# Optimization experiments

Hardware: AMD Instinct MI355X
Metric: run time of the kernel (lower is better)

Reference implementation:

```python
import jax, jax.numpy as jnp
import numpy as np

B, L, C = 32, 8192, 32
P, S = 16, 8
N = (L - P) // S + 1  # 1023 tokens
K = 16
HID = max(16, 2 * K)  # 32
STD_FLOOR = 0.01


def setup_inputs() -> dict:
    key = jax.random.key(0)
    ks = jax.random.split(key, 8)
    return {
        "x": jax.random.normal(ks[0], (B, L, C), jnp.float32),
        "freq_features": jax.random.normal(ks[1], (B * C, N, K), jnp.float32),
        "alpha_w1": jax.random.normal(ks[2], (K, HID), jnp.float32) * 0.1,
        "alpha_b1": jnp.zeros((HID,), jnp.float32),
        "alpha_w2": jax.random.normal(ks[3], (HID, 1), jnp.float32) * 0.1,
        "alpha_b2": jnp.zeros((1,), jnp.float32),
        "beta_w1": jax.random.normal(ks[4], (K, HID), jnp.float32) * 0.1,
        "beta_b1": jnp.zeros((HID,), jnp.float32),
        "beta_w2": jax.random.normal(ks[5], (HID, 1), jnp.float32) * 0.1,
        "beta_b2": jnp.zeros((1,), jnp.float32),
        "affine_scale": jnp.ones((C,), jnp.float32),
        "affine_bias": jnp.zeros((C,), jnp.float32),
        "n_tokens": N,
    }


def _gate_mlp(ff, w1, b1, w2, b2):
    # Linear -> exact GELU (torch default) -> Linear -> sigmoid, squeeze last dim
    h = jax.nn.gelu(ff @ w1 + b1, approximate=False)
    return jax.nn.sigmoid((h @ w2 + b2)[..., 0])


def reference(x, freq_features, alpha_w1, alpha_b1, alpha_w2, alpha_b2,
              beta_w1, beta_b1, beta_w2, beta_b2, affine_scale, affine_bias,
              n_tokens):
    Bx, Lx, Cx = x.shape
    Nn = n_tokens
    # global stats over time dim (biased var)
    mu_g = jnp.mean(x, axis=1, keepdims=True)                     # [B,1,C]
    var_g = jnp.mean((x - mu_g) ** 2, axis=1, keepdims=True)
    std_g = jnp.sqrt(jnp.maximum(var_g, STD_FLOOR * STD_FLOOR))
    # local per-patch stats via strided gather (equivalent to unfold)
    idx = jnp.arange(Nn)[:, None] * S + jnp.arange(P)[None, :]    # [N,P]
    patches = x[:, idx, :]                                        # [B,N,P,C]
    mu_l = jnp.mean(patches, axis=2)                              # [B,N,C]
    var_l = jnp.mean((patches - mu_l[:, :, None, :]) ** 2, axis=2)
    std_l = jnp.sqrt(jnp.maximum(var_l, STD_FLOOR * STD_FLOOR))   # [B,N,C]
    # map each timestep to nearest patch center
    centers = jnp.arange(Nn, dtype=jnp.float32) * S + P / 2.0
    dist = jnp.abs(jnp.arange(Lx, dtype=jnp.float32)[:, None] - centers[None, :])
    tok_per_time = jnp.argmin(dist, axis=1)                       # [L] int
    mu_l_t = mu_l[:, tok_per_time, :]                             # [B,L,C]
    std_l_t = std_l[:, tok_per_time, :]
    # freq-conditioned mixing gate alpha per token, gathered per timestep
    ff = freq_features.reshape(Bx, Cx, Nn, -1)                    # [B,C,N,K]
    alpha_tok = _gate_mlp(ff, alpha_w1, alpha_b1, alpha_w2, alpha_b2)  # [B,C,N]
    beta_tok = _gate_mlp(ff, beta_w1, beta_b1, beta_w2, beta_b2)       # [B,C,N] (ctx only)
    alpha_t = jnp.transpose(alpha_tok[:, :, tok_per_time], (0, 2, 1))  # [B,L,C]
    # normalize and mix
    x_norm_local = jnp.clip((x - mu_l_t) / jnp.maximum(std_l_t, STD_FLOOR), -30.0, 30.0)
    x_norm_global = jnp.clip((x - mu_g) / jnp.maximum(std_g, STD_FLOOR), -30.0, 30.0)
    x_norm = alpha_t * x_norm_local + (1.0 - alpha_t) * x_norm_global
    x_norm = x_norm * affine_scale[None, None, :] + affine_bias[None, None, :]
    return x_norm
```

## Files before the change

kernel.cpp:

```cpp
#include <hip/hip_runtime.h>
#include <math.h>

#define BB   32
#define LL   8192
#define CC   32
#define NTOK 1023
#define KK   16
#define HID  32

typedef short  bf16x8 __attribute__((ext_vector_type(8)));
typedef float  f32x4v __attribute__((ext_vector_type(4)));
typedef unsigned int u32;
typedef unsigned short ushort_t;

__device__ __forceinline__ float4 f4add(float4 a, float4 b) {
    return make_float4(a.x + b.x, a.y + b.y, a.z + b.z, a.w + b.w);
}
__device__ __forceinline__ float4 f4fma(float4 a, float4 b, float4 c) {
    return make_float4(fmaf(a.x, b.x, c.x), fmaf(a.y, b.y, c.y),
                       fmaf(a.z, b.z, c.z), fmaf(a.w, b.w, c.w));
}
__device__ __forceinline__ float4 shflx4(float4 v, int m) {
    return make_float4(__shfl_xor(v.x, m, 64), __shfl_xor(v.y, m, 64),
                       __shfl_xor(v.z, m, 64), __shfl_xor(v.w, m, 64));
}
__device__ __forceinline__ float ex2(float x) {
    return __builtin_amdgcn_exp2f(x);
}
__device__ __forceinline__ u32 pkbf16(float a, float b) {
    u32 r;
    asm("v_cvt_pk_bf16_f32 %0, %1, %2" : "=v"(r) : "v"(a), "v"(b));
    return r;
}


__global__ void __launch_bounds__(256)
kA_fused(const float* __restrict__ x,  const float* __restrict__ ff,
         const float* __restrict__ w1g, const float* __restrict__ b1,
         const float* __restrict__ w2,  const float* __restrict__ b2,
         float* __restrict__ ps, float* __restrict__ pq,
         float* __restrict__ mu_l, float* __restrict__ rstd_l,
         float* __restrict__ alpha_t) {
    __shared__ float4 smem4[592];
    int t   = threadIdx.x;
    int idx = blockIdx.x;
    int r3  = idx % 3, q3 = idx / 3;

    if (r3 == 0) {
        float4* part_s = smem4;
        float4* part_q = part_s + 256;
        float4* halo_s = part_q + 256;
        float4* halo_q = halo_s + 8;
        float4* wred_s = halo_q + 8;
        float4* wred_q = wred_s + 32;

        int b  = q3 >> 5;
        int s  = q3 & 31;
        int c4 = t & 7, rgrp = t >> 3;
        const float4* xb = (const float4*)x + ((size_t)b * LL + s * 256) * 8;

        float4 v[8];
#pragma unroll
        for (int k = 0; k < 8; ++k)
            v[k] = xb[(rgrp * 8 + k) * 8 + c4];
        float4 s4 = make_float4(0.f, 0.f, 0.f, 0.f);
        float4 q4 = make_float4(0.f, 0.f, 0.f, 0.f);
#pragma unroll
        for (int k = 0; k < 8; ++k) {
            s4 = f4add(s4, v[k]);
            q4 = f4fma(v[k], v[k], q4);
        }
        part_s[t] = s4;
        part_q[t] = q4;

        if (t < 64) {
            float4 hs = make_float4(0.f, 0.f, 0.f, 0.f);
            float4 hq = make_float4(0.f, 0.f, 0.f, 0.f);
            if (s < 31) {
                float4 hv = xb[(256 + (t >> 3)) * 8 + c4];
                hs = hv; hq = f4fma(hv, hv, hq);
            }
            hs = f4add(hs, shflx4(hs, 8));  hq = f4add(hq, shflx4(hq, 8));
            hs = f4add(hs, shflx4(hs, 16)); hq = f4add(hq, shflx4(hq, 16));
            hs = f4add(hs, shflx4(hs, 32)); hq = f4add(hq, shflx4(hq, 32));
            if (t < 8) { halo_s[t] = hs; halo_q[t] = hq; }
        }

        float4 gs = s4, gq = q4;
        gs = f4add(gs, shflx4(gs, 8));  gq = f4add(gq, shflx4(gq, 8));
        gs = f4add(gs, shflx4(gs, 16)); gq = f4add(gq, shflx4(gq, 16));
        gs = f4add(gs, shflx4(gs, 32)); gq = f4add(gq, shflx4(gq, 32));
        if ((t & 56) == 0) {
            wred_s[(t >> 6) * 8 + c4] = gs;
            wred_q[(t >> 6) * 8 + c4] = gq;
        }
        __syncthreads();

        int nl = t >> 3;
        int n  = s * 32 + nl;
        if (n < NTOK) {
            float4 a  = (nl < 31) ? part_s[(nl + 1) * 8 + c4] : halo_s[c4];
            float4 bq = (nl < 31) ? part_q[(nl + 1) * 8 + c4] : halo_q[c4];
            float4 ts = f4add(part_s[t], a);
            float4 tq = f4add(part_q[t], bq);
            float4 mu = make_float4(ts.x * 0.0625f, ts.y * 0.0625f,
                                    ts.z * 0.0625f, ts.w * 0.0625f);
            float4 var;
            var.x = fmaxf(fmaf(-mu.x, mu.x, tq.x * 0.0625f), 1e-4f);
            var.y = fmaxf(fmaf(-mu.y, mu.y, tq.y * 0.0625f), 1e-4f);
            var.z = fmaxf(fmaf(-mu.z, mu.z, tq.z * 0.0625f), 1e-4f);
            var.w = fmaxf(fmaf(-mu.w, mu.w, tq.w * 0.0625f), 1e-4f);
            float4 rs = make_float4(1.f / sqrtf(var.x), 1.f / sqrtf(var.y),
                                    1.f / sqrtf(var.z), 1.f / sqrtf(var.w));
            size_t o = (size_t)(b * NTOK + n) * 8 + c4;
            ((float4*)mu_l)[o]   = mu;
            ((float4*)rstd_l)[o] = rs;
        }

        if (t < 8) {
            float4 a = f4add(f4add(wred_s[t], wred_s[8 + t]),
                             f4add(wred_s[16 + t], wred_s[24 + t]));
            float4 c = f4add(f4add(wred_q[t], wred_q[8 + t]),
                             f4add(wred_q[16 + t], wred_q[24 + t]));
            ((float4*)ps)[q3 * 8 + t] = a;
            ((float4*)pq)[q3 * 8 + t] = c;
        }
    } else {
        float* als = (float*)smem4;
        int a_id = q3 * 2 + (r3 - 1);
        int b    = a_id >> 6;
        int n0   = (a_id & 63) * 16;
        int l  = t & 63, wv = t >> 6;
        bool active = (l < 32);

        int kb = 8 * ((l >> 4) & 1);
        int j0 = l & 15;
        union { u32 w[4]; bf16x8 v; } UA0, UA1;
#pragma unroll
        for (int p = 0; p < 4; ++p) {
            float a0 = w1g[(kb + 2*p)     * HID + j0];
            float a1 = w1g[(kb + 2*p + 1) * HID + j0];
            float a2 = w1g[(kb + 2*p)     * HID + j0 + 16];
            float a3 = w1g[(kb + 2*p + 1) * HID + j0 + 16];
            u32 u0 = pkbf16(a0, a1), u1 = pkbf16(a2, a3);
            UA0.w[p] = active ? u0 : 0u;
            UA1.w[p] = active ? u1 : 0u;
        }
        bf16x8 Alo = UA0.v, Ahi = UA1.v;

        int jg = 4 * (l >> 4);
        f32x4v b1lo = *(const f32x4v*)(b1 + jg);
        f32x4v b1hi = *(const f32x4v*)(b1 + 16 + jg);
        f32x4v w2lo = *(const f32x4v*)(w2 + jg);
        f32x4v w2hi = *(const f32x4v*)(w2 + 16 + jg);
        float b2s = b2[0];

        const float C0 = -2.302211325f;
        const float C1 = -0.102943702f;

        int nlane = min(n0 + (l & 15), NTOK - 1);
        size_t cbase = (size_t)(b * 32 + 8 * wv) * NTOK;
        const float4* fpc = (const float4*)ff + (cbase + nlane) * 4
                          + ((l >> 4) & 1) * 2;
        const int STRD = NTOK * 4;

        float4 a0 = fpc[0],     a1 = fpc[1];
        float4 p0 = fpc[STRD],  p1 = fpc[STRD + 1];

        for (int it = 0; it < 8; ++it) {
            float4 f0 = a0, f1 = a1;
            a0 = p0; a1 = p1;
            if (it < 6) { p0 = fpc[2 * STRD]; p1 = fpc[2 * STRD + 1]; }
            fpc += STRD;

            union { u32 w[4]; bf16x8 v; } B;
            u32 w0 = pkbf16(f0.x, f0.y), w1v = pkbf16(f0.z, f0.w);
            u32 w2v = pkbf16(f1.x, f1.y), w3 = pkbf16(f1.z, f1.w);
            B.w[0] = active ? w0 : 0u;  B.w[1] = active ? w1v : 0u;
            B.w[2] = active ? w2v : 0u; B.w[3] = active ? w3 : 0u;

            f32x4v d0 = __builtin_amdgcn_mfma_f32_16x16x32_bf16(Alo, B.v, b1lo, 0, 0, 0);
            f32x4v d1 = __builtin_amdgcn_mfma_f32_16x16x32_bf16(Ahi, B.v, b1hi, 0, 0, 0);

            float partial = 0.f;
#pragma unroll
            for (int r = 0; r < 4; ++r) {
                float h  = d0[r];
                float a  = fmaf(h * h, C1, C0);
                float g  = h * __builtin_amdgcn_rcpf(1.0f + ex2(a * h));
                partial  = fmaf(g, w2lo[r], partial);
                float h2 = d1[r];
                float a2 = fmaf(h2 * h2, C1, C0);
                float g2 = h2 * __builtin_amdgcn_rcpf(1.0f + ex2(a2 * h2));
                partial  = fmaf(g2, w2hi[r], partial);
            }
            partial += __shfl_xor(partial, 16, 64);
            partial += __shfl_xor(partial, 32, 64);
            float outv = b2s + partial;
            float av = __builtin_amdgcn_rcpf(1.0f + ex2(-1.44269504f * outv));
            if (l < 16) als[(8 * wv + it) * 17 + l] = av;
        }
        __syncthreads();

        int flat = t * 2;
        int nn = flat >> 5, cc = flat & 31;
        if (n0 + nn < NTOK) {
            float2 o;
            o.x = als[cc * 17 + nn];
            o.y = als[(cc + 1) * 17 + nn];
            *(float2*)(alpha_t + ((size_t)(b * NTOK + n0 + nn)) * CC + cc) = o;
        }
    }
}

__global__ void __launch_bounds__(256)
k4_main(const float4* __restrict__ x4,
        const float* __restrict__ ps, const float* __restrict__ pq,
        const float4* __restrict__ mul4, const float4* __restrict__ rsl4,
        const float4* __restrict__ al4,
        const float4* __restrict__ sc4, const float4* __restrict__ bi4,
        float4* __restrict__ out4) {
    __shared__ float red_s[8][32], red_q[8][32];
    __shared__ float mugs[32], rsgs[32];
    int t  = threadIdx.x;
    int i4 = blockIdx.x * 256 + t;
    int b  = i4 >> 16;

    {
        int c = t & 31, grp = t >> 5;
        float s = 0.f, q = 0.f;
#pragma unroll
        for (int i = 0; i < 4; ++i) {
            int sl = grp * 4 + i;
            s += ps[(b * 32 + sl) * 32 + c];
            q += pq[(b * 32 + sl) * 32 + c];
        }
        red_s[grp][c] = s; red_q[grp][c] = q;
        __syncthreads();
        if (t < 32) {
            float ss = 0.f, qq = 0.f;
#pragma unroll
            for (int g = 0; g < 8; ++g) { ss += red_s[g][t]; qq += red_q[g][t]; }
            float mu  = ss * (1.0f / LL);
            float var = fmaxf(qq * (1.0f / LL) - mu * mu, 1e-4f);
            mugs[t] = mu;
            rsgs[t] = 1.0f / sqrtf(var);
        }
        __syncthreads();
    }

    int c4 = i4 & 7;
    int l  = (i4 >> 3) & (LL - 1);
    int n  = (l >= 5) ? min((l - 5) >> 3, NTOK - 1) : 0;

    float4 xv = x4[i4];
    float4 mg = *(const float4*)(mugs + 4 * c4);
    float4 rg = *(const float4*)(rsgs + 4 * c4);
    int o4 = (b * NTOK + n) * 8 + c4;
    float4 ml = mul4[o4], rl = rsl4[o4], av = al4[o4];
    float4 s  = sc4[c4],  bi = bi4[c4];

    float4 y;
    {
        float xg = fminf(fmaxf((xv.x - mg.x) * rg.x, -30.f), 30.f);
        float xl = fminf(fmaxf((xv.x - ml.x) * rl.x, -30.f), 30.f);
        y.x = fmaf(av.x, xl - xg, xg) * s.x + bi.x;
    }
    {
        float xg = fminf(fmaxf((xv.y - mg.y) * rg.y, -30.f), 30.f);
        float xl = fminf(fmaxf((xv.y - ml.y) * rl.y, -30.f), 30.f);
        y.y = fmaf(av.y, xl - xg, xg) * s.y + bi.y;
    }
    {
        float xg = fminf(fmaxf((xv.z - mg.z) * rg.z, -30.f), 30.f);
        float xl = fminf(fmaxf((xv.z - ml.z) * rl.z, -30.f), 30.f);
        y.z = fmaf(av.z, xl - xg, xg) * s.z + bi.z;
    }
    {
        float xg = fminf(fmaxf((xv.w - mg.w) * rg.w, -30.f), 30.f);
        float xl = fminf(fmaxf((xv.w - ml.w) * rl.w, -30.f), 30.f);
        y.w = fmaf(av.w, xl - xg, xg) * s.w + bi.w;
    }
    out4[i4] = y;
}

extern "C" void kernel_launch(void* const* d_in, const int* in_sizes, int n_in,
                              void* d_out, int out_size, void* d_ws, size_t ws_size,
                              hipStream_t stream) {
    const float* x    = (const float*)d_in[0];
    const float* ff   = (const float*)d_in[1];
    const float* aw1  = (const float*)d_in[2];
    const float* ab1  = (const float*)d_in[3];
    const float* aw2  = (const float*)d_in[4];
    const float* ab2  = (const float*)d_in[5];
    const float* scal = (const float*)d_in[10];
    const float* bias = (const float*)d_in[11];
    float* out = (float*)d_out;

    float* wsf     = (float*)d_ws;
    float* ps      = wsf;
    float* pq      = wsf + 32768;
    float* mu_l    = wsf + 65536;
    float* rstd_l  = mu_l    + 1047552;
    float* alpha_t = rstd_l  + 1047552;

    kA_fused<<<3072, 256, 0, stream>>>(x, ff, aw1, ab1, aw2, ab2,
                                       ps, pq, mu_l, rstd_l, alpha_t);
    k4_main<<<8192, 256, 0, stream>>>((const float4*)x, ps, pq,
                                      (const float4*)mu_l, (const float4*)rstd_l,
                                      (const float4*)alpha_t,
                                      (const float4*)scal, (const float4*)bias,
                                      (float4*)out);
}
```

Measured before the change: 41.83 us.

## Use 32x32x16 MFMA for gate MLP with 32 tokens per block

The alpha gate MLP path switches from two 16x16x32 bf16 MFMAs, where half the lanes were masked idle, to a single 32x32x16 MFMA. All 64 lanes now carry data and each block covers 32 tokens instead of 16. The stats and gate block roles now alternate even/odd, shrinking the fused grid from 3072 to 2048 blocks, and the alpha write-out uses float4 stores. This removes wasted lanes and per-block overhead in the gate path, at the cost of more registers for the 16-wide accumulator and GELU loop.

```diff
diff --git a/kernel.cpp b/kernel.cpp
--- a/kernel.cpp
+++ b/kernel.cpp
@@ -10,8 +10,8 @@
 
 typedef short  bf16x8 __attribute__((ext_vector_type(8)));
 typedef float  f32x4v __attribute__((ext_vector_type(4)));
+typedef float  f32x16 __attribute__((ext_vector_type(16)));
 typedef unsigned int u32;
-typedef unsigned short ushort_t;
 
 __device__ __forceinline__ float4 f4add(float4 a, float4 b) {
     return make_float4(a.x + b.x, a.y + b.y, a.z + b.z, a.w + b.w);
@@ -44,9 +44,9 @@
     __shared__ float4 smem4[592];
     int t   = threadIdx.x;
     int idx = blockIdx.x;
-    int r3  = idx % 3, q3 = idx / 3;
-
-    if (r3 == 0) {
+
+    if ((idx & 1) == 0) {
+        int q = idx >> 1;
         float4* part_s = smem4;
         float4* part_q = part_s + 256;
         float4* halo_s = part_q + 256;
@@ -54,8 +54,8 @@
         float4* wred_s = halo_q + 8;
         float4* wred_q = wred_s + 32;
 
-        int b  = q3 >> 5;
-        int s  = q3 & 31;
+        int b  = q >> 5;
+        int s  = q & 31;
         int c4 = t & 7, rgrp = t >> 3;
         const float4* xb = (const float4*)x + ((size_t)b * LL + s * 256) * 8;
 
@@ -122,46 +122,47 @@
                              f4add(wred_s[16 + t], wred_s[24 + t]));
             float4 c = f4add(f4add(wred_q[t], wred_q[8 + t]),
                              f4add(wred_q[16 + t], wred_q[24 + t]));
-            ((float4*)ps)[q3 * 8 + t] = a;
-            ((float4*)pq)[q3 * 8 + t] = c;
+            ((float4*)ps)[q * 8 + t] = a;
+            ((float4*)pq)[q * 8 + t] = c;
         }
     } else {
         float* als = (float*)smem4;
-        int a_id = q3 * 2 + (r3 - 1);
-        int b    = a_id >> 6;
-        int n0   = (a_id & 63) * 16;
+        int a_id = idx >> 1;
+        int b    = a_id >> 5;
+        int n0   = (a_id & 31) * 32;
         int l  = t & 63, wv = t >> 6;
-        bool active = (l < 32);
-
-        int kb = 8 * ((l >> 4) & 1);
-        int j0 = l & 15;
-        union { u32 w[4]; bf16x8 v; } UA0, UA1;
+        int kh = l >> 5;
+
+        int j0 = l & 31;
+        union { u32 w[4]; bf16x8 v; } UA;
 #pragma unroll
         for (int p = 0; p < 4; ++p) {
-            float a0 = w1g[(kb + 2*p)     * HID + j0];
-            float a1 = w1g[(kb + 2*p + 1) * HID + j0];
-            float a2 = w1g[(kb + 2*p)     * HID + j0 + 16];
-            float a3 = w1g[(kb + 2*p + 1) * HID + j0 + 16];
-            u32 u0 = pkbf16(a0, a1), u1 = pkbf16(a2, a3);
-            UA0.w[p] = active ? u0 : 0u;
-            UA1.w[p] = active ? u1 : 0u;
-        }
-        bf16x8 Alo = UA0.v, Ahi = UA1.v;
-
-        int jg = 4 * (l >> 4);
-        f32x4v b1lo = *(const f32x4v*)(b1 + jg);
-        f32x4v b1hi = *(const f32x4v*)(b1 + 16 + jg);
-        f32x4v w2lo = *(const f32x4v*)(w2 + jg);
-        f32x4v w2hi = *(const f32x4v*)(w2 + 16 + jg);
+            float a0 = w1g[(8 * kh + 2*p)     * HID + j0];
+            float a1 = w1g[(8 * kh + 2*p + 1) * HID + j0];
+            UA.w[p] = pkbf16(a0, a1);
+        }
+        bf16x8 A = UA.v;
+
+        f32x16 cfrag;
+        float  w2f[16];
+#pragma unroll
+        for (int g = 0; g < 4; ++g) {
+            f32x4v bb = *(const f32x4v*)(b1 + 8 * g + 4 * kh);
+            f32x4v ww = *(const f32x4v*)(w2 + 8 * g + 4 * kh);
+#pragma unroll
+            for (int r = 0; r < 4; ++r) {
+                cfrag[g * 4 + r] = bb[r];
+                w2f [g * 4 + r] = ww[r];
+            }
+        }
         float b2s = b2[0];
 
         const float C0 = -2.302211325f;
         const float C1 = -0.102943702f;
 
-        int nlane = min(n0 + (l & 15), NTOK - 1);
+        int nlane = min(n0 + (l & 31), NTOK - 1);
         size_t cbase = (size_t)(b * 32 + 8 * wv) * NTOK;
-        const float4* fpc = (const float4*)ff + (cbase + nlane) * 4
-                          + ((l >> 4) & 1) * 2;
+        const float4* fpc = (const float4*)ff + (cbase + nlane) * 4 + kh * 2;
         const int STRD = NTOK * 4;
 
         float4 a0 = fpc[0],     a1 = fpc[1];
@@ -174,41 +175,35 @@
             fpc += STRD;
 
             union { u32 w[4]; bf16x8 v; } B;
-            u32 w0 = pkbf16(f0.x, f0.y), w1v = pkbf16(f0.z, f0.w);
-            u32 w2v = pkbf16(f1.x, f1.y), w3 = pkbf16(f1.z, f1.w);
-            B.w[0] = active ? w0 : 0u;  B.w[1] = active ? w1v : 0u;
-            B.w[2] = active ? w2v : 0u; B.w[3] = active ? w3 : 0u;
-
-            f32x4v d0 = __builtin_amdgcn_mfma_f32_16x16x32_bf16(Alo, B.v, b1lo, 0, 0, 0);
-            f32x4v d1 = __builtin_amdgcn_mfma_f32_16x16x32_bf16(Ahi, B.v, b1hi, 0, 0, 0);
+            B.w[0] = pkbf16(f0.x, f0.y); B.w[1] = pkbf16(f0.z, f0.w);
+            B.w[2] = pkbf16(f1.x, f1.y); B.w[3] = pkbf16(f1.z, f1.w);
+
+            f32x16 d = __builtin_amdgcn_mfma_f32_32x32x16_bf16(A, B.v, cfrag, 0, 0, 0);
 
             float partial = 0.f;
 #pragma unroll
-            for (int r = 0; r < 4; ++r) {
-                float h  = d0[r];
-                float a  = fmaf(h * h, C1, C0);
-                float g  = h * __builtin_amdgcn_rcpf(1.0f + ex2(a * h));
-                partial  = fmaf(g, w2lo[r], partial);
-                float h2 = d1[r];
-                float a2 = fmaf(h2 * h2, C1, C0);
-                float g2 = h2 * __builtin_amdgcn_rcpf(1.0f + ex2(a2 * h2));
-                partial  = fmaf(g2, w2hi[r], partial);
+            for (int r = 0; r < 16; ++r) {
+                float h = d[r];
+                float a = fmaf(h * h, C1, C0);
+                float g = h * __builtin_amdgcn_rcpf(1.0f + ex2(a * h));
+                partial = fmaf(g, w2f[r], partial);
             }
-            partial += __shfl_xor(partial, 16, 64);
             partial += __shfl_xor(partial, 32, 64);
             float outv = b2s + partial;
             float av = __builtin_amdgcn_rcpf(1.0f + ex2(-1.44269504f * outv));
-            if (l < 16) als[(8 * wv + it) * 17 + l] = av;
+            if (l < 32) als[(8 * wv + it) * 33 + l] = av;
         }
         __syncthreads();
 
-        int flat = t * 2;
-        int nn = flat >> 5, cc = flat & 31;
+        int nn  = t >> 3;
+        int cc0 = (t & 7) * 4;
         if (n0 + nn < NTOK) {
-            float2 o;
-            o.x = als[cc * 17 + nn];
-            o.y = als[(cc + 1) * 17 + nn];
-            *(float2*)(alpha_t + ((size_t)(b * NTOK + n0 + nn)) * CC + cc) = o;
+            float4 o;
+            o.x = als[(cc0    ) * 33 + nn];
+            o.y = als[(cc0 + 1) * 33 + nn];
+            o.z = als[(cc0 + 2) * 33 + nn];
+            o.w = als[(cc0 + 3) * 33 + nn];
+            *(float4*)(alpha_t + ((size_t)(b * NTOK + n0 + nn)) * CC + cc0) = o;
         }
     }
 }
@@ -304,7 +299,7 @@
     float* rstd_l  = mu_l    + 1047552;
     float* alpha_t = rstd_l  + 1047552;
 
-    kA_fused<<<3072, 256, 0, stream>>>(x, ff, aw1, ab1, aw2, ab2,
+    kA_fused<<<2048, 256, 0, stream>>>(x, ff, aw1, ab1, aw2, ab2,
                                        ps, pq, mu_l, rstd_l, alpha_t);
     k4_main<<<8192, 256, 0, stream>>>((const float4*)x, ps, pq,
                                       (const float4*)mu_l, (const float4*)rstd_l,
```

Measured after the change: 47.18 us. 12.8% more time.
